# Kernel optimization log

Hardware: AMD Instinct MI355X
Metric: run time of the kernel (lower is better)

## Reference

```python
import jax, jax.numpy as jnp
import numpy as np

N = 20000      # nodes
E = 320000     # edges (avg degree 16)
H = 256        # hidden_dim
COORD = 3      # 3D coordinates
LN_EPS = 1e-5


def setup_inputs() -> dict:
    key = jax.random.key(0)
    ks = jax.random.split(key, 16)
    def w(k, shape, fan_in):
        return (jax.random.normal(k, shape, jnp.float32) / np.sqrt(fan_in)).astype(jnp.float32)
    return {
        "h": jax.random.normal(ks[0], (N, H), jnp.float32),
        "x": jax.random.normal(ks[1], (N, COORD), jnp.float32),
        "edge_index": jax.random.randint(ks[2], (2, E), 0, N, dtype=jnp.int64),
        # edge_mlp: Linear(2H+1 -> H), SiLU, Linear(H -> H), SiLU
        "e_w1": w(ks[3], (2 * H + 1, H), 2 * H + 1), "e_b1": jnp.zeros((H,), jnp.float32),
        "e_w2": w(ks[4], (H, H), H),                 "e_b2": jnp.zeros((H,), jnp.float32),
        # coord_mlp: Linear(H -> H), SiLU, Linear(H -> 1, no bias)
        "c_w1": w(ks[5], (H, H), H),                 "c_b1": jnp.zeros((H,), jnp.float32),
        "c_w2": w(ks[6], (H, 1), H),
        # node_mlp: Linear(2H -> H), SiLU, Linear(H -> H)
        "n_w1": w(ks[7], (2 * H, H), 2 * H),         "n_b1": jnp.zeros((H,), jnp.float32),
        "n_w2": w(ks[8], (H, H), H),                 "n_b2": jnp.zeros((H,), jnp.float32),
        # LayerNorm
        "ln_g": jnp.ones((H,), jnp.float32),         "ln_b": jnp.zeros((H,), jnp.float32),
    }


def reference(h, x, edge_index, e_w1, e_b1, e_w2, e_b2,
              c_w1, c_b1, c_w2, n_w1, n_b1, n_w2, n_b2, ln_g, ln_b):
    n_nodes = h.shape[0]
    row, col = edge_index[0], edge_index[1]

    diff = x[row] - x[col]                                    # [E, 3]
    dist_sq = jnp.sum(diff * diff, axis=-1, keepdims=True)    # [E, 1]
    edge_input = jnp.concatenate([h[row], h[col], dist_sq], axis=-1)  # [E, 2H+1]

    m = jax.nn.silu(edge_input @ e_w1 + e_b1)
    m_ij = jax.nn.silu(m @ e_w2 + e_b2)                        # [E, H]

    coord_weight = jax.nn.silu(m_ij @ c_w1 + c_b1) @ c_w2     # [E, 1]
    coord_agg = jax.ops.segment_sum(coord_weight * diff, col, num_segments=n_nodes)
    x_new = x + coord_agg                                     # [N, 3]

    msg_agg = jax.ops.segment_sum(m_ij, col, num_segments=n_nodes)  # [N, H]
    h_cat = jnp.concatenate([h, msg_agg], axis=-1)            # [N, 2H]
    h_new = jax.nn.silu(h_cat @ n_w1 + n_b1) @ n_w2 + n_b2

    y = h + h_new
    mu = jnp.mean(y, axis=-1, keepdims=True)
    var = jnp.mean((y - mu) ** 2, axis=-1, keepdims=True)
    h_out = (y - mu) * jax.lax.rsqrt(var + LN_EPS) * ln_g + ln_b
    return (h_out, x_new)
```

## Files before the change

kernel.cpp:

```cpp
#include <hip/hip_runtime.h>
#include <hip/hip_fp16.h>
#include <math.h>

#define NN 20000
#define NE 320000
#define H 256
#define LN_EPS 1e-5f
#define TE 64

typedef _Float16 f16x8 __attribute__((ext_vector_type(8)));
typedef float f32x16 __attribute__((ext_vector_type(16)));

__device__ __forceinline__ float silu1(float v) {
    return __fdividef(v, 1.0f + __expf(-v));
}

__device__ __forceinline__ __half2 silu2(const __half2 s) {
    const __half2 one2 = __float2half2_rn(1.0f);
    return __hmul2(s, h2rcp(__hadd2(one2, h2exp(__hneg2(s)))));
}

__global__ __launch_bounds__(256) void k_misc(
    const int* __restrict__ ei, int* __restrict__ bins,
    const float* __restrict__ x, float* __restrict__ xout,
    const float* __restrict__ ew2, const float* __restrict__ cw1,
    const float* __restrict__ nw2, const float* __restrict__ nw1,
    const float* __restrict__ ew1,
    _Float16* __restrict__ Bp2, _Float16* __restrict__ Bp3,
    _Float16* __restrict__ BpB, _Float16* __restrict__ BpA,
    _Float16* __restrict__ Bp1, _Float16* __restrict__ wdh,
    float* __restrict__ msg) {
    const int b = blockIdx.x;
    const int tid = threadIdx.x;
    if (b < 1250) {
        atomicAdd(&bins[ei[NE + b * 256 + tid]], 1);
    } else if (b < 1485) {
        const int i = (b - 1250) * 256 + tid;
        if (i < NN * 3) xout[i] = x[i];
    } else if (b < 2125) {
        const int pb = b - 1485;
        const int which = pb >> 7;
        const int bx = pb & 127;
        const int n = tid;
        if (which < 3) {
            if (bx >= 64) return;
            const float* W = (which == 0) ? ew2 : (which == 1) ? cw1 : nw2;
            _Float16* Bp = (which == 0) ? Bp2 : (which == 1) ? Bp3 : BpB;
            #pragma unroll
            for (int kr = 0; kr < 4; kr++) {
                const int k = bx * 4 + kr;
                Bp[((size_t)(k >> 3) * 256 + n) * 8 + (k & 7)] =
                    (_Float16)W[(size_t)k * 256 + n];
            }
        } else if (which == 3) {
            #pragma unroll
            for (int kr = 0; kr < 4; kr++) {
                const int k = bx * 4 + kr;
                BpA[((size_t)(k >> 3) * 256 + n) * 8 + (k & 7)] =
                    (_Float16)nw1[(size_t)k * 256 + n];
            }
        } else {
            if (bx >= 64) return;
            #pragma unroll
            for (int kr = 0; kr < 4; kr++) {
                const int k = bx * 4 + kr;
                Bp1[((size_t)(k >> 3) * 512 + n) * 8 + (k & 7)] =
                    (_Float16)ew1[(size_t)k * 256 + n];
                Bp1[((size_t)(k >> 3) * 512 + 256 + n) * 8 + (k & 7)] =
                    (_Float16)ew1[(size_t)(256 + k) * 256 + n];
            }
        }
    } else if (b == 2125) {
        wdh[tid] = (_Float16)ew1[(size_t)512 * H + tid];
    } else {
        const int b2 = b - 2126;
        float4* m4 = (float4*)msg;
        const float4 z = make_float4(0.f, 0.f, 0.f, 0.f);
        #pragma unroll
        for (int k = 0; k < 4; k++)
            m4[(size_t)b2 * 256 + tid + (size_t)k * 320000] = z;
    }
}

__global__ __launch_bounds__(256, 4) void k_pre(const float* __restrict__ h,
                                                const _Float16* __restrict__ Bp1,
                                                const float* __restrict__ eb1,
                                                _Float16* __restrict__ P,
                                                _Float16* __restrict__ Q,
                                                const int* __restrict__ bins,
                                                int* __restrict__ cursor) {
    __shared__ f16x8 Ap[32 * 32];
    const int tid = threadIdx.x;

    if (blockIdx.x == NN / 32) {
        __shared__ int wsum2[4];
        __shared__ int wbase2[4];
        const int lane = tid & 63;
        const int wid = tid >> 6;
        const int base = tid * 79;
        int sum = 0;
        for (int j = 0; j < 79; j++) {
            const int idx = base + j;
            sum += (idx < NN) ? bins[idx] : 0;
        }
        int inc = sum;
        #pragma unroll
        for (int off = 1; off < 64; off <<= 1) {
            const int t = __shfl_up(inc, off);
            if (lane >= off) inc += t;
        }
        if (lane == 63) wsum2[wid] = inc;
        __syncthreads();
        if (tid == 0) {
            int r = 0;
            #pragma unroll
            for (int ww = 0; ww < 4; ww++) { wbase2[ww] = r; r += wsum2[ww]; }
        }
        __syncthreads();
        int run = wbase2[wid] + inc - sum;
        for (int j = 0; j < 79; j++) {
            const int idx = base + j;
            if (idx < NN) { const int v = bins[idx]; cursor[idx] = run; run += v; }
        }
        return;
    }

    const int l = tid & 63;
    const int w = tid >> 6;
    const int l31 = l & 31;
    const int hh = l >> 5;
    const int n0 = blockIdx.x * 32;

    {
        const int kb = tid & 31;
        const int eb = tid >> 5;
        #pragma unroll
        for (int i = 0; i < 4; i++) {
            const int e = eb + i * 8;
            const float4 v0 = *(const float4*)(h + (size_t)(n0 + e) * H + kb * 8);
            const float4 v1 = *(const float4*)(h + (size_t)(n0 + e) * H + kb * 8 + 4);
            f16x8 pk;
            pk[0] = (_Float16)v0.x; pk[1] = (_Float16)v0.y;
            pk[2] = (_Float16)v0.z; pk[3] = (_Float16)v0.w;
            pk[4] = (_Float16)v1.x; pk[5] = (_Float16)v1.y;
            pk[6] = (_Float16)v1.z; pk[7] = (_Float16)v1.w;
            Ap[kb * 32 + (e ^ (kb & 7))] = pk;
        }
    }
    __syncthreads();

    const f16x8* Bv = (const f16x8*)Bp1;
    f32x16 acc[4];
    #pragma unroll
    for (int nt = 0; nt < 4; nt++)
        #pragma unroll
        for (int r = 0; r < 16; r++) acc[nt][r] = 0.0f;

    #pragma unroll 4
    for (int kk = 0; kk < 16; kk++) {
        const int kb = kk * 2 + hh;
        const f16x8 a = Ap[kb * 32 + (l31 ^ (kb & 7))];
        #pragma unroll
        for (int nt = 0; nt < 4; nt++) {
            const f16x8 bfr = Bv[(size_t)kb * 512 + w * 128 + nt * 32 + l31];
            acc[nt] = __builtin_amdgcn_mfma_f32_32x32x16_f16(a, bfr, acc[nt], 0, 0, 0);
        }
    }

    #pragma unroll
    for (int nt = 0; nt < 4; nt++) {
        const int col = w * 128 + nt * 32 + l31;
        const float bias = (col < 256) ? eb1[col] : 0.0f;
        #pragma unroll
        for (int r = 0; r < 16; r++) {
            const int node = n0 + (r & 3) + 8 * (r >> 2) + 4 * hh;
            const float v = acc[nt][r] + bias;
            if (col < 256) P[(size_t)node * H + col] = (_Float16)v;
            else           Q[(size_t)node * H + col - 256] = (_Float16)v;
        }
    }
}

__global__ void k_scatter(const int* __restrict__ ei, int* __restrict__ cursor,
                          int* __restrict__ perm) {
    const int e = blockIdx.x * blockDim.x + threadIdx.x;
    if (e < NE) {
        const int c = ei[NE + e];
        const int pos = atomicAdd(&cursor[c], 1);
        perm[pos] = e;
    }
}

__global__ __launch_bounds__(256, 4) void k_edge(
    const float* __restrict__ x, const int* __restrict__ ei,
    const int* __restrict__ perm,
    const _Float16* __restrict__ P, const _Float16* __restrict__ Q,
    const _Float16* __restrict__ wdh,
    const _Float16* __restrict__ Bp2, const float* __restrict__ eb2,
    const _Float16* __restrict__ Bp3, const float* __restrict__ cb1,
    const float* __restrict__ cw2,
    float* __restrict__ msg, float* __restrict__ xout) {
    __shared__ f16x8 Ap[32 * 64];
    __shared__ float sdiff[TE][4];
    __shared__ int srow[TE];
    __shared__ int scol[TE];
    __shared__ float scw[TE];

    const int tid = threadIdx.x;
    const int e0blk = blockIdx.x * TE;
    const int l = tid & 63;
    const int w = tid >> 6;
    const int l31 = l & 31;
    const int hh = l >> 5;

    if (tid < TE) {
        const int e = perm[e0blk + tid];
        const int r = ei[e];
        const int c = ei[NE + e];
        const float dx = x[r * 3 + 0] - x[c * 3 + 0];
        const float dy = x[r * 3 + 1] - x[c * 3 + 1];
        const float dz = x[r * 3 + 2] - x[c * 3 + 2];
        srow[tid] = r; scol[tid] = c;
        sdiff[tid][0] = dx; sdiff[tid][1] = dy; sdiff[tid][2] = dz;
        sdiff[tid][3] = dx * dx + dy * dy + dz * dz;
        scw[tid] = 0.0f;
    }
    __syncthreads();

    {
        const f16x8* Pv = (const f16x8*)P;
        const f16x8* Qv = (const f16x8*)Q;
        const int kb = tid & 31;
        const int eb = tid >> 5;
        union { f16x8 v; __half2 h[4]; } wdu;
        wdu.v = ((const f16x8*)wdh)[kb];
        #pragma unroll 4
        for (int i = 0; i < 8; i++) {
            const int e = eb + i * 8;
            const __half2 d2 = __float2half2_rn(sdiff[e][3]);
            union { f16x8 v; __half2 h[4]; } pu, qu, su;
            pu.v = Pv[(size_t)srow[e] * 32 + kb];
            qu.v = Qv[(size_t)scol[e] * 32 + kb];
            #pragma unroll
            for (int j = 0; j < 4; j++) {
                const __half2 s = __hfma2(wdu.h[j], d2, __hadd2(pu.h[j], qu.h[j]));
                su.h[j] = silu2(s);
            }
            Ap[kb * 64 + (e ^ (kb & 7))] = su.v;
        }
    }
    __syncthreads();

    const f16x8* Bp2v = (const f16x8*)Bp2;
    const f16x8* Bp3v = (const f16x8*)Bp3;

    f32x16 acc0[2], acc1[2];
    #pragma unroll
    for (int nt = 0; nt < 2; nt++)
        #pragma unroll
        for (int r = 0; r < 16; r++) { acc0[nt][r] = 0.0f; acc1[nt][r] = 0.0f; }

    #pragma unroll 4
    for (int kk = 0; kk < 16; kk++) {
        const int kb = kk * 2 + hh;
        const f16x8 a0 = Ap[kb * 64 + (l31 ^ (kb & 7))];
        const f16x8 a1 = Ap[kb * 64 + ((32 + l31) ^ (kb & 7))];
        #pragma unroll
        for (int nt = 0; nt < 2; nt++) {
            const f16x8 b = Bp2v[(size_t)kb * 256 + w * 64 + nt * 32 + l31];
            acc0[nt] = __builtin_amdgcn_mfma_f32_32x32x16_f16(a0, b, acc0[nt], 0, 0, 0);
            acc1[nt] = __builtin_amdgcn_mfma_f32_32x32x16_f16(a1, b, acc1[nt], 0, 0, 0);
        }
    }

    __syncthreads();

    {
        __half* Aph = (__half*)Ap;
        #pragma unroll
        for (int nt = 0; nt < 2; nt++) {
            const int c = w * 64 + nt * 32 + l31;
            const float bias = eb2[c];
            const int kb2 = c >> 3;
            const int j = c & 7;
            #pragma unroll
            for (int r = 0; r < 16; r++) {
                const __half2 o = silu2(__floats2half2_rn(acc0[nt][r] + bias,
                                                          acc1[nt][r] + bias));
                const int e0 = (r & 3) + 8 * (r >> 2) + 4 * hh;
                Aph[(size_t)(kb2 * 64 + (e0 ^ (kb2 & 7))) * 8 + j] = __low2half(o);
                Aph[(size_t)(kb2 * 64 + ((e0 + 32) ^ (kb2 & 7))) * 8 + j] = __high2half(o);
            }
        }
    }
    __syncthreads();

    #pragma unroll
    for (int nt = 0; nt < 2; nt++)
        #pragma unroll
        for (int r = 0; r < 16; r++) { acc0[nt][r] = 0.0f; acc1[nt][r] = 0.0f; }

    #pragma unroll 4
    for (int kk = 0; kk < 16; kk++) {
        const int kb = kk * 2 + hh;
        const f16x8 a0 = Ap[kb * 64 + (l31 ^ (kb & 7))];
        const f16x8 a1 = Ap[kb * 64 + ((32 + l31) ^ (kb & 7))];
        #pragma unroll
        for (int nt = 0; nt < 2; nt++) {
            const f16x8 b = Bp3v[(size_t)kb * 256 + w * 64 + nt * 32 + l31];
            acc0[nt] = __builtin_amdgcn_mfma_f32_32x32x16_f16(a0, b, acc0[nt], 0, 0, 0);
            acc1[nt] = __builtin_amdgcn_mfma_f32_32x32x16_f16(a1, b, acc1[nt], 0, 0, 0);
        }
    }

    {
        __half2 p[16];
        #pragma unroll
        for (int r = 0; r < 16; r++) p[r] = __float2half2_rn(0.0f);
        #pragma unroll
        for (int nt = 0; nt < 2; nt++) {
            const int c = w * 64 + nt * 32 + l31;
            const float bias = cb1[c];
            const __half2 cwv = __float2half2_rn(cw2[c]);
            #pragma unroll
            for (int r = 0; r < 16; r++) {
                const __half2 s = __floats2half2_rn(acc0[nt][r] + bias,
                                                    acc1[nt][r] + bias);
                p[r] = __hfma2(silu2(s), cwv, p[r]);
            }
        }
        #pragma unroll
        for (int m = 1; m < 32; m <<= 1) {
            #pragma unroll
            for (int r = 0; r < 16; r++) {
                union { __half2 h; int i; } u, v;
                u.h = p[r];
                v.i = __shfl_xor(u.i, m);
                p[r] = __hadd2(u.h, v.h);
            }
        }
        if (l31 == 0) {
            #pragma unroll
            for (int r = 0; r < 16; r++) {
                const int e0 = (r & 3) + 8 * (r >> 2) + 4 * hh;
                atomicAdd(&scw[e0], __low2float(p[r]));
                atomicAdd(&scw[e0 + 32], __high2float(p[r]));
            }
        }
    }
    __syncthreads();

    {
        const _Float16* Apf = (const _Float16*)Ap;
        const int c = tid;
        const int kb = c >> 3;
        const int j = c & 7;
        float accm = 0.0f;
        #pragma unroll 4
        for (int e = 0; e < TE; e++) {
            accm += (float)Apf[(size_t)(kb * 64 + (e ^ (kb & 7))) * 8 + j];
            const int col = scol[e];
            const int nxt = (e == TE - 1) ? -1 : scol[e + 1];
            if (col != nxt) {
                atomicAdd(msg + (size_t)col * H + c, accm);
                accm = 0.0f;
            }
        }
    }

    if (tid < 3) {
        const int d = tid;
        float accc = 0.0f;
        for (int e = 0; e < TE; e++) {
            accc += scw[e] * sdiff[e][d];
            const int col = scol[e];
            const int nxt = (e == TE - 1) ? -1 : scol[e + 1];
            if (col != nxt) {
                atomicAdd(xout + (size_t)col * 3 + d, accc);
                accc = 0.0f;
            }
        }
    }
}

__global__ __launch_bounds__(256, 4) void k_node(
    const float* __restrict__ h, const float* __restrict__ msg,
    const _Float16* __restrict__ BpA, const float* __restrict__ nb1,
    const _Float16* __restrict__ BpB, const float* __restrict__ nb2,
    const float* __restrict__ lng, const float* __restrict__ lnb,
    float* __restrict__ hout) {
    __shared__ f16x8 ApA[64 * 32];
    __shared__ float s1[32];
    __shared__ float s2[32];
    f16x8* Tp = ApA;
    const int tid = threadIdx.x;
    const int l = tid & 63;
    const int w = tid >> 6;
    const int l31 = l & 31;
    const int hh = l >> 5;
    const int n0 = blockIdx.x * 32;

    if (tid < 32) { s1[tid] = 0.0f; s2[tid] = 0.0f; }

    {
        const int kb = tid & 31;
        const int eb = tid >> 5;
        #pragma unroll
        for (int i = 0; i < 4; i++) {
            const int e = eb + i * 8;
            #pragma unroll
            for (int half = 0; half < 2; half++) {
                const float* A = half ? msg : h;
                const int kb2 = kb + half * 32;
                const float4 v0 = *(const float4*)(A + (size_t)(n0 + e) * H + kb * 8);
                const float4 v1 = *(const float4*)(A + (size_t)(n0 + e) * H + kb * 8 + 4);
                f16x8 pk;
                pk[0] = (_Float16)v0.x; pk[1] = (_Float16)v0.y;
                pk[2] = (_Float16)v0.z; pk[3] = (_Float16)v0.w;
                pk[4] = (_Float16)v1.x; pk[5] = (_Float16)v1.y;
                pk[6] = (_Float16)v1.z; pk[7] = (_Float16)v1.w;
                ApA[kb2 * 32 + (e ^ (kb2 & 7))] = pk;
            }
        }
    }
    __syncthreads();

    const f16x8* BvA = (const f16x8*)BpA;
    const f16x8* BvB = (const f16x8*)BpB;

    f32x16 acc[2];
    #pragma unroll
    for (int nt = 0; nt < 2; nt++)
        #pragma unroll
        for (int r = 0; r < 16; r++) acc[nt][r] = 0.0f;

    #pragma unroll 4
    for (int kk = 0; kk < 32; kk++) {
        const int kb = kk * 2 + hh;
        const f16x8 a = ApA[kb * 32 + (l31 ^ (kb & 7))];
        #pragma unroll
        for (int nt = 0; nt < 2; nt++) {
            const f16x8 b = BvA[(size_t)kb * 256 + w * 64 + nt * 32 + l31];
            acc[nt] = __builtin_amdgcn_mfma_f32_32x32x16_f16(a, b, acc[nt], 0, 0, 0);
        }
    }
    __syncthreads();

    {
        _Float16* Tpf = (_Float16*)Tp;
        #pragma unroll
        for (int nt = 0; nt < 2; nt++) {
            const int col = w * 64 + nt * 32 + l31;
            const float bias = nb1[col];
            const int kb2 = col >> 3;
            const int j = col & 7;
            #pragma unroll
            for (int r = 0; r < 16; r++) {
                const int e = (r & 3) + 8 * (r >> 2) + 4 * hh;
                Tpf[(size_t)(kb2 * 32 + (e ^ (kb2 & 7))) * 8 + j] =
                    (_Float16)silu1(acc[nt][r] + bias);
            }
        }
    }
    __syncthreads();

    f32x16 y[2];
    #pragma unroll
    for (int nt = 0; nt < 2; nt++)
        #pragma unroll
        for (int r = 0; r < 16; r++) y[nt][r] = 0.0f;

    #pragma unroll 4
    for (int kk = 0; kk < 16; kk++) {
        const int kb = kk * 2 + hh;
        const f16x8 a = Tp[kb * 32 + (l31 ^ (kb & 7))];
        #pragma unroll
        for (int nt = 0; nt < 2; nt++) {
            const f16x8 b = BvB[(size_t)kb * 256 + w * 64 + nt * 32 + l31];
            y[nt] = __builtin_amdgcn_mfma_f32_32x32x16_f16(a, b, y[nt], 0, 0, 0);
        }
    }

    float t1[16], t2[16];
    #pragma unroll
    for (int r = 0; r < 16; r++) { t1[r] = 0.0f; t2[r] = 0.0f; }
    #pragma unroll
    for (int nt = 0; nt < 2; nt++) {
        const int col = w * 64 + nt * 32 + l31;
        const float bias = nb2[col];
        #pragma unroll
        for (int r = 0; r < 16; r++) {
            const int node = n0 + (r & 3) + 8 * (r >> 2) + 4 * hh;
            const float v = y[nt][r] + bias + h[(size_t)node * H + col];
            y[nt][r] = v;
            t1[r] += v;
            t2[r] += v * v;
        }
    }
    #pragma unroll
    for (int m = 1; m < 32; m <<= 1) {
        #pragma unroll
        for (int r = 0; r < 16; r++) {
            t1[r] += __shfl_xor(t1[r], m);
            t2[r] += __shfl_xor(t2[r], m);
        }
    }
    if (l31 == 0) {
        #pragma unroll
        for (int r = 0; r < 16; r++) {
            const int row = (r & 3) + 8 * (r >> 2) + 4 * hh;
            atomicAdd(&s1[row], t1[r]);
            atomicAdd(&s2[row], t2[r]);
        }
    }
    __syncthreads();

    #pragma unroll
    for (int nt = 0; nt < 2; nt++) {
        const int col = w * 64 + nt * 32 + l31;
        const float g = lng[col];
        const float bb = lnb[col];
        #pragma unroll
        for (int r = 0; r < 16; r++) {
            const int row = (r & 3) + 8 * (r >> 2) + 4 * hh;
            const int node = n0 + row;
            const float mu = s1[row] * (1.0f / H);
            const float var = s2[row] * (1.0f / H) - mu * mu;
            const float rs = rsqrtf(var + LN_EPS);
            hout[(size_t)node * H + col] = (y[nt][r] - mu) * rs * g + bb;
        }
    }
}

extern "C" void kernel_launch(void* const* d_in, const int* in_sizes, int n_in,
                              void* d_out, int out_size, void* d_ws, size_t ws_size,
                              hipStream_t stream) {
    const float* h   = (const float*)d_in[0];
    const float* x   = (const float*)d_in[1];
    const int*   ei  = (const int*)d_in[2];
    const float* ew1 = (const float*)d_in[3];
    const float* eb1 = (const float*)d_in[4];
    const float* ew2 = (const float*)d_in[5];
    const float* eb2 = (const float*)d_in[6];
    const float* cw1 = (const float*)d_in[7];
    const float* cb1 = (const float*)d_in[8];
    const float* cw2 = (const float*)d_in[9];
    const float* nw1 = (const float*)d_in[10];
    const float* nb1 = (const float*)d_in[11];
    const float* nw2 = (const float*)d_in[12];
    const float* nb2 = (const float*)d_in[13];
    const float* lng = (const float*)d_in[14];
    const float* lnb = (const float*)d_in[15];

    float* hout = (float*)d_out;
    float* xout = hout + (size_t)NN * H;

    float* msg = (float*)d_ws;
    int* bins = (int*)(msg + (size_t)NN * H);
    _Float16* P   = (_Float16*)(bins + NN);
    _Float16* Qq  = P + (size_t)NN * H;
    _Float16* Bp2 = Qq + (size_t)NN * H;
    _Float16* Bp3 = Bp2 + 256 * 256;
    _Float16* BpB = Bp3 + 256 * 256;
    _Float16* BpA = BpB + 256 * 256;
    _Float16* Bp1 = BpA + 512 * 256;
    _Float16* wdh = Bp1 + 256 * 512;
    int* cursor = (int*)(wdh + 256);
    int* perm   = cursor + NN;

    (void)hipMemsetAsync(bins, 0, (size_t)NN * 4, stream);
    k_misc<<<3376, 256, 0, stream>>>(ei, bins, x, xout, ew2, cw1, nw2, nw1, ew1,
                                     Bp2, Bp3, BpB, BpA, Bp1, wdh, msg);
    k_pre<<<NN / 32 + 1, 256, 0, stream>>>(h, Bp1, eb1, P, Qq, bins, cursor);
    k_scatter<<<(NE + 255) / 256, 256, 0, stream>>>(ei, cursor, perm);
    k_edge<<<NE / TE, 256, 0, stream>>>(x, ei, perm, P, Qq, wdh, Bp2, eb2,
                                        Bp3, cb1, cw2, msg, xout);
    k_node<<<NN / 32, 256, 0, stream>>>(h, msg, BpA, nb1, BpB, nb2,
                                        lng, lnb, hout);
}
```

Measured before the change: 373.3 us.

## Merge all stages into one persistent cooperative kernel with grid syncs

Replaces the five separate launches (misc prep, pre-projection, scatter, edge, node) with a single cooperative persistent kernel. Blocks grid-stride over each former stage's work, with grid.sync between stages. The aim is to remove per-launch overhead and inter-kernel gaps. In exchange it adds grid-wide barriers, caps the grid at the occupancy-derived size (at most 1024 blocks), and forces one shared-memory and register budget that must fit the largest stage, which may lower occupancy.

```diff
diff --git a/kernel.cpp b/kernel.cpp
--- a/kernel.cpp
+++ b/kernel.cpp
@@ -1,6 +1,9 @@
 #include <hip/hip_runtime.h>
 #include <hip/hip_fp16.h>
+#include <hip/hip_cooperative_groups.h>
 #include <math.h>
+
+namespace cg = cooperative_groups;
 
 #define NN 20000
 #define NE 320000
@@ -20,514 +23,499 @@
     return __hmul2(s, h2rcp(__hadd2(one2, h2exp(__hneg2(s)))));
 }
 
-__global__ __launch_bounds__(256) void k_misc(
-    const int* __restrict__ ei, int* __restrict__ bins,
-    const float* __restrict__ x, float* __restrict__ xout,
-    const float* __restrict__ ew2, const float* __restrict__ cw1,
-    const float* __restrict__ nw2, const float* __restrict__ nw1,
-    const float* __restrict__ ew1,
-    _Float16* __restrict__ Bp2, _Float16* __restrict__ Bp3,
-    _Float16* __restrict__ BpB, _Float16* __restrict__ BpA,
-    _Float16* __restrict__ Bp1, _Float16* __restrict__ wdh,
-    float* __restrict__ msg) {
-    const int b = blockIdx.x;
+struct MegaParams {
+    const int* ei; int* bins;
+    const float* x; float* xout;
+    const float* ew2; const float* cw1; const float* nw2; const float* nw1;
+    const float* ew1;
+    _Float16 *Bp2, *Bp3, *BpB, *BpA, *Bp1, *wdh;
+    float* msg;
+    const float* h; const float* eb1;
+    _Float16 *P, *Q;
+    int* cursor; int* perm;
+    const float *eb2, *cb1, *cw2;
+    const float *nb1, *nb2, *lng, *lnb;
+    float* hout;
+};
+
+__global__ __launch_bounds__(256, 4) void k_mega(MegaParams p) {
+    cg::grid_group grid = cg::this_grid();
     const int tid = threadIdx.x;
-    if (b < 1250) {
-        atomicAdd(&bins[ei[NE + b * 256 + tid]], 1);
-    } else if (b < 1485) {
-        const int i = (b - 1250) * 256 + tid;
-        if (i < NN * 3) xout[i] = x[i];
-    } else if (b < 2125) {
-        const int pb = b - 1485;
-        const int which = pb >> 7;
-        const int bx = pb & 127;
-        const int n = tid;
-        if (which < 3) {
-            if (bx >= 64) return;
-            const float* W = (which == 0) ? ew2 : (which == 1) ? cw1 : nw2;
-            _Float16* Bp = (which == 0) ? Bp2 : (which == 1) ? Bp3 : BpB;
-            #pragma unroll
-            for (int kr = 0; kr < 4; kr++) {
-                const int k = bx * 4 + kr;
-                Bp[((size_t)(k >> 3) * 256 + n) * 8 + (k & 7)] =
-                    (_Float16)W[(size_t)k * 256 + n];
-            }
-        } else if (which == 3) {
-            #pragma unroll
-            for (int kr = 0; kr < 4; kr++) {
-                const int k = bx * 4 + kr;
-                BpA[((size_t)(k >> 3) * 256 + n) * 8 + (k & 7)] =
-                    (_Float16)nw1[(size_t)k * 256 + n];
-            }
-        } else {
-            if (bx >= 64) return;
-            #pragma unroll
-            for (int kr = 0; kr < 4; kr++) {
-                const int k = bx * 4 + kr;
-                Bp1[((size_t)(k >> 3) * 512 + n) * 8 + (k & 7)] =
-                    (_Float16)ew1[(size_t)k * 256 + n];
-                Bp1[((size_t)(k >> 3) * 512 + 256 + n) * 8 + (k & 7)] =
-                    (_Float16)ew1[(size_t)(256 + k) * 256 + n];
-            }
-        }
-    } else if (b == 2125) {
-        wdh[tid] = (_Float16)ew1[(size_t)512 * H + tid];
-    } else {
-        const int b2 = b - 2126;
-        float4* m4 = (float4*)msg;
-        const float4 z = make_float4(0.f, 0.f, 0.f, 0.f);
-        #pragma unroll
-        for (int k = 0; k < 4; k++)
-            m4[(size_t)b2 * 256 + tid + (size_t)k * 320000] = z;
-    }
-}
-
-__global__ __launch_bounds__(256, 4) void k_pre(const float* __restrict__ h,
-                                                const _Float16* __restrict__ Bp1,
-                                                const float* __restrict__ eb1,
-                                                _Float16* __restrict__ P,
-                                                _Float16* __restrict__ Q,
-                                                const int* __restrict__ bins,
-                                                int* __restrict__ cursor) {
-    __shared__ f16x8 Ap[32 * 32];
-    const int tid = threadIdx.x;
-
-    if (blockIdx.x == NN / 32) {
-        __shared__ int wsum2[4];
-        __shared__ int wbase2[4];
-        const int lane = tid & 63;
-        const int wid = tid >> 6;
-        const int base = tid * 79;
-        int sum = 0;
-        for (int j = 0; j < 79; j++) {
-            const int idx = base + j;
-            sum += (idx < NN) ? bins[idx] : 0;
-        }
-        int inc = sum;
-        #pragma unroll
-        for (int off = 1; off < 64; off <<= 1) {
-            const int t = __shfl_up(inc, off);
-            if (lane >= off) inc += t;
-        }
-        if (lane == 63) wsum2[wid] = inc;
-        __syncthreads();
-        if (tid == 0) {
-            int r = 0;
-            #pragma unroll
-            for (int ww = 0; ww < 4; ww++) { wbase2[ww] = r; r += wsum2[ww]; }
-        }
-        __syncthreads();
-        int run = wbase2[wid] + inc - sum;
-        for (int j = 0; j < 79; j++) {
-            const int idx = base + j;
-            if (idx < NN) { const int v = bins[idx]; cursor[idx] = run; run += v; }
-        }
-        return;
-    }
+    const int nB = gridDim.x;
+
+    __shared__ f16x8 ApS[2048];
+    __shared__ float sdiff[TE][4];
+    __shared__ int srow[TE];
+    __shared__ int scol[TE];
+    __shared__ float scw[TE];
+    __shared__ float s1[32];
+    __shared__ float s2[32];
+    __shared__ int wsum2[4];
+    __shared__ int wbase2[4];
 
     const int l = tid & 63;
     const int w = tid >> 6;
     const int l31 = l & 31;
     const int hh = l >> 5;
-    const int n0 = blockIdx.x * 32;
-
-    {
-        const int kb = tid & 31;
-        const int eb = tid >> 5;
-        #pragma unroll
-        for (int i = 0; i < 4; i++) {
-            const int e = eb + i * 8;
-            const float4 v0 = *(const float4*)(h + (size_t)(n0 + e) * H + kb * 8);
-            const float4 v1 = *(const float4*)(h + (size_t)(n0 + e) * H + kb * 8 + 4);
-            f16x8 pk;
-            pk[0] = (_Float16)v0.x; pk[1] = (_Float16)v0.y;
-            pk[2] = (_Float16)v0.z; pk[3] = (_Float16)v0.w;
-            pk[4] = (_Float16)v1.x; pk[5] = (_Float16)v1.y;
-            pk[6] = (_Float16)v1.z; pk[7] = (_Float16)v1.w;
-            Ap[kb * 32 + (e ^ (kb & 7))] = pk;
+
+    for (int b = blockIdx.x; b < 3376; b += nB) {
+        if (b < 1250) {
+            atomicAdd(&p.bins[p.ei[NE + b * 256 + tid]], 1);
+        } else if (b < 1485) {
+            const int i = (b - 1250) * 256 + tid;
+            if (i < NN * 3) p.xout[i] = p.x[i];
+        } else if (b < 2125) {
+            const int pb = b - 1485;
+            const int which = pb >> 7;
+            const int bx = pb & 127;
+            const int n = tid;
+            if (which < 3) {
+                if (bx < 64) {
+                    const float* W = (which == 0) ? p.ew2 : (which == 1) ? p.cw1 : p.nw2;
+                    _Float16* Bp = (which == 0) ? p.Bp2 : (which == 1) ? p.Bp3 : p.BpB;
+                    #pragma unroll
+                    for (int kr = 0; kr < 4; kr++) {
+                        const int k = bx * 4 + kr;
+                        Bp[((size_t)(k >> 3) * 256 + n) * 8 + (k & 7)] =
+                            (_Float16)W[(size_t)k * 256 + n];
+                    }
+                }
+            } else if (which == 3) {
+                #pragma unroll
+                for (int kr = 0; kr < 4; kr++) {
+                    const int k = bx * 4 + kr;
+                    p.BpA[((size_t)(k >> 3) * 256 + n) * 8 + (k & 7)] =
+                        (_Float16)p.nw1[(size_t)k * 256 + n];
+                }
+            } else {
+                if (bx < 64) {
+                    #pragma unroll
+                    for (int kr = 0; kr < 4; kr++) {
+                        const int k = bx * 4 + kr;
+                        p.Bp1[((size_t)(k >> 3) * 512 + n) * 8 + (k & 7)] =
+                            (_Float16)p.ew1[(size_t)k * 256 + n];
+                        p.Bp1[((size_t)(k >> 3) * 512 + 256 + n) * 8 + (k & 7)] =
+                            (_Float16)p.ew1[(size_t)(256 + k) * 256 + n];
+                    }
+                }
+            }
+        } else if (b == 2125) {
+            p.wdh[tid] = (_Float16)p.ew1[(size_t)512 * H + tid];
+        } else {
+            const int b2 = b - 2126;
+            float4* m4 = (float4*)p.msg;
+            const float4 z = make_float4(0.f, 0.f, 0.f, 0.f);
+            #pragma unroll
+            for (int k = 0; k < 4; k++)
+                m4[(size_t)b2 * 256 + tid + (size_t)k * 320000] = z;
         }
     }
-    __syncthreads();
-
-    const f16x8* Bv = (const f16x8*)Bp1;
-    f32x16 acc[4];
-    #pragma unroll
-    for (int nt = 0; nt < 4; nt++)
-        #pragma unroll
-        for (int r = 0; r < 16; r++) acc[nt][r] = 0.0f;
-
-    #pragma unroll 4
-    for (int kk = 0; kk < 16; kk++) {
-        const int kb = kk * 2 + hh;
-        const f16x8 a = Ap[kb * 32 + (l31 ^ (kb & 7))];
-        #pragma unroll
-        for (int nt = 0; nt < 4; nt++) {
-            const f16x8 bfr = Bv[(size_t)kb * 512 + w * 128 + nt * 32 + l31];
-            acc[nt] = __builtin_amdgcn_mfma_f32_32x32x16_f16(a, bfr, acc[nt], 0, 0, 0);
+    grid.sync();
+
+    for (int t = blockIdx.x; t <= 625; t += nB) {
+        __syncthreads();
+        if (t == 625) {
+            const int lane = tid & 63;
+            const int wid = tid >> 6;
+            const int base = tid * 79;
+            int sum = 0;
+            for (int j = 0; j < 79; j++) {
+                const int idx = base + j;
+                sum += (idx < NN) ? p.bins[idx] : 0;
+            }
+            int inc = sum;
+            #pragma unroll
+            for (int off = 1; off < 64; off <<= 1) {
+                const int tt = __shfl_up(inc, off);
+                if (lane >= off) inc += tt;
+            }
+            if (lane == 63) wsum2[wid] = inc;
+            __syncthreads();
+            if (tid == 0) {
+                int r = 0;
+                #pragma unroll
+                for (int ww = 0; ww < 4; ww++) { wbase2[ww] = r; r += wsum2[ww]; }
+            }
+            __syncthreads();
+            int run = wbase2[wid] + inc - sum;
+            for (int j = 0; j < 79; j++) {
+                const int idx = base + j;
+                if (idx < NN) { const int v = p.bins[idx]; p.cursor[idx] = run; run += v; }
+            }
+        } else {
+            f16x8* Ap = ApS;
+            const int n0 = t * 32;
+            {
+                const int kb = tid & 31;
+                const int eb = tid >> 5;
+                #pragma unroll
+                for (int i = 0; i < 4; i++) {
+                    const int e = eb + i * 8;
+                    const float4 v0 = *(const float4*)(p.h + (size_t)(n0 + e) * H + kb * 8);
+                    const float4 v1 = *(const float4*)(p.h + (size_t)(n0 + e) * H + kb * 8 + 4);
+                    f16x8 pk;
+                    pk[0] = (_Float16)v0.x; pk[1] = (_Float16)v0.y;
+                    pk[2] = (_Float16)v0.z; pk[3] = (_Float16)v0.w;
+                    pk[4] = (_Float16)v1.x; pk[5] = (_Float16)v1.y;
+                    pk[6] = (_Float16)v1.z; pk[7] = (_Float16)v1.w;
+                    Ap[kb * 32 + (e ^ (kb & 7))] = pk;
+                }
+            }
+            __syncthreads();
+
+            const f16x8* Bv = (const f16x8*)p.Bp1;
+            f32x16 acc[4];
+            #pragma unroll
+            for (int nt = 0; nt < 4; nt++)
+                #pragma unroll
+                for (int r = 0; r < 16; r++) acc[nt][r] = 0.0f;
+
+            #pragma unroll 4
+            for (int kk = 0; kk < 16; kk++) {
+                const int kb = kk * 2 + hh;
+                const f16x8 a = Ap[kb * 32 + (l31 ^ (kb & 7))];
+                #pragma unroll
+                for (int nt = 0; nt < 4; nt++) {
+                    const f16x8 bfr = Bv[(size_t)kb * 512 + w * 128 + nt * 32 + l31];
+                    acc[nt] = __builtin_amdgcn_mfma_f32_32x32x16_f16(a, bfr, acc[nt], 0, 0, 0);
+                }
+            }
+
+            #pragma unroll
+            for (int nt = 0; nt < 4; nt++) {
+                const int col = w * 128 + nt * 32 + l31;
+                const float bias = (col < 256) ? p.eb1[col] : 0.0f;
+                #pragma unroll
+                for (int r = 0; r < 16; r++) {
+                    const int node = n0 + (r & 3) + 8 * (r >> 2) + 4 * hh;
+                    const float v = acc[nt][r] + bias;
+                    if (col < 256) p.P[(size_t)node * H + col] = (_Float16)v;
+                    else           p.Q[(size_t)node * H + col - 256] = (_Float16)v;
+                }
+            }
         }
     }
-
-    #pragma unroll
-    for (int nt = 0; nt < 4; nt++) {
-        const int col = w * 128 + nt * 32 + l31;
-        const float bias = (col < 256) ? eb1[col] : 0.0f;
-        #pragma unroll
-        for (int r = 0; r < 16; r++) {
-            const int node = n0 + (r & 3) + 8 * (r >> 2) + 4 * hh;
-            const float v = acc[nt][r] + bias;
-            if (col < 256) P[(size_t)node * H + col] = (_Float16)v;
-            else           Q[(size_t)node * H + col - 256] = (_Float16)v;
-        }
+    grid.sync();
+
+    for (int u = blockIdx.x; u < 1250; u += nB) {
+        const int e = u * 256 + tid;
+        const int c = p.ei[NE + e];
+        const int pos = atomicAdd(&p.cursor[c], 1);
+        p.perm[pos] = e;
     }
-}
-
-__global__ void k_scatter(const int* __restrict__ ei, int* __restrict__ cursor,
-                          int* __restrict__ perm) {
-    const int e = blockIdx.x * blockDim.x + threadIdx.x;
-    if (e < NE) {
-        const int c = ei[NE + e];
-        const int pos = atomicAdd(&cursor[c], 1);
-        perm[pos] = e;
+    grid.sync();
+
+    for (int t = blockIdx.x; t < NE / TE; t += nB) {
+        __syncthreads();
+        f16x8* Ap = ApS;
+        const int e0blk = t * TE;
+
+        if (tid < TE) {
+            const int e = p.perm[e0blk + tid];
+            const int r = p.ei[e];
+            const int c = p.ei[NE + e];
+            const float dx = p.x[r * 3 + 0] - p.x[c * 3 + 0];
+            const float dy = p.x[r * 3 + 1] - p.x[c * 3 + 1];
+            const float dz = p.x[r * 3 + 2] - p.x[c * 3 + 2];
+            srow[tid] = r; scol[tid] = c;
+            sdiff[tid][0] = dx; sdiff[tid][1] = dy; sdiff[tid][2] = dz;
+            sdiff[tid][3] = dx * dx + dy * dy + dz * dz;
+            scw[tid] = 0.0f;
+        }
+        __syncthreads();
+
+        {
+            const f16x8* Pv = (const f16x8*)p.P;
+            const f16x8* Qv = (const f16x8*)p.Q;
+            const int kb = tid & 31;
+            const int eb = tid >> 5;
+            union { f16x8 v; __half2 h[4]; } wdu;
+            wdu.v = ((const f16x8*)p.wdh)[kb];
+            #pragma unroll 4
+            for (int i = 0; i < 8; i++) {
+                const int e = eb + i * 8;
+                const __half2 d2 = __float2half2_rn(sdiff[e][3]);
+                union { f16x8 v; __half2 h[4]; } pu, qu, su;
+                pu.v = Pv[(size_t)srow[e] * 32 + kb];
+                qu.v = Qv[(size_t)scol[e] * 32 + kb];
+                #pragma unroll
+                for (int j = 0; j < 4; j++) {
+                    const __half2 s = __hfma2(wdu.h[j], d2, __hadd2(pu.h[j], qu.h[j]));
+                    su.h[j] = silu2(s);
+                }
+                Ap[kb * 64 + (e ^ (kb & 7))] = su.v;
+            }
+        }
+        __syncthreads();
+
+        const f16x8* Bp2v = (const f16x8*)p.Bp2;
+        const f16x8* Bp3v = (const f16x8*)p.Bp3;
+
+        f32x16 acc0[2], acc1[2];
+        #pragma unroll
+        for (int nt = 0; nt < 2; nt++)
+            #pragma unroll
+            for (int r = 0; r < 16; r++) { acc0[nt][r] = 0.0f; acc1[nt][r] = 0.0f; }
+
+        #pragma unroll 4
+        for (int kk = 0; kk < 16; kk++) {
+            const int kb = kk * 2 + hh;
+            const f16x8 a0 = Ap[kb * 64 + (l31 ^ (kb & 7))];
+            const f16x8 a1 = Ap[kb * 64 + ((32 + l31) ^ (kb & 7))];
+            #pragma unroll
+            for (int nt = 0; nt < 2; nt++) {
+                const f16x8 b = Bp2v[(size_t)kb * 256 + w * 64 + nt * 32 + l31];
+                acc0[nt] = __builtin_amdgcn_mfma_f32_32x32x16_f16(a0, b, acc0[nt], 0, 0, 0);
+                acc1[nt] = __builtin_amdgcn_mfma_f32_32x32x16_f16(a1, b, acc1[nt], 0, 0, 0);
+            }
+        }
+
+        __syncthreads();
+
+        {
+            __half* Aph = (__half*)Ap;
+            #pragma unroll
+            for (int nt = 0; nt < 2; nt++) {
+                const int c = w * 64 + nt * 32 + l31;
+                const float bias = p.eb2[c];
+                const int kb2 = c >> 3;
+                const int j = c & 7;
+                #pragma unroll
+                for (int r = 0; r < 16; r++) {
+                    const __half2 o = silu2(__floats2half2_rn(acc0[nt][r] + bias,
+                                                              acc1[nt][r] + bias));
+                    const int e0 = (r & 3) + 8 * (r >> 2) + 4 * hh;
+                    Aph[(size_t)(kb2 * 64 + (e0 ^ (kb2 & 7))) * 8 + j] = __low2half(o);
+                    Aph[(size_t)(kb2 * 64 + ((e0 + 32) ^ (kb2 & 7))) * 8 + j] = __high2half(o);
+                }
+            }
+        }
+        __syncthreads();
+
+        #pragma unroll
+        for (int nt = 0; nt < 2; nt++)
+            #pragma unroll
+            for (int r = 0; r < 16; r++) { acc0[nt][r] = 0.0f; acc1[nt][r] = 0.0f; }
+
+        #pragma unroll 4
+        for (int kk = 0; kk < 16; kk++) {
+            const int kb = kk * 2 + hh;
+            const f16x8 a0 = Ap[kb * 64 + (l31 ^ (kb & 7))];
+            const f16x8 a1 = Ap[kb * 64 + ((32 + l31) ^ (kb & 7))];
+            #pragma unroll
+            for (int nt = 0; nt < 2; nt++) {
+                const f16x8 b = Bp3v[(size_t)kb * 256 + w * 64 + nt * 32 + l31];
+                acc0[nt] = __builtin_amdgcn_mfma_f32_32x32x16_f16(a0, b, acc0[nt], 0, 0, 0);
+                acc1[nt] = __builtin_amdgcn_mfma_f32_32x32x16_f16(a1, b, acc1[nt], 0, 0, 0);
+            }
+        }
+
+        {
+            __half2 pr[16];
+            #pragma unroll
+            for (int r = 0; r < 16; r++) pr[r] = __float2half2_rn(0.0f);
+            #pragma unroll
+            for (int nt = 0; nt < 2; nt++) {
+                const int c = w * 64 + nt * 32 + l31;
+                const float bias = p.cb1[c];
+                const __half2 cwv = __float2half2_rn(p.cw2[c]);
+                #pragma unroll
+                for (int r = 0; r < 16; r++) {
+                    const __half2 s = __floats2half2_rn(acc0[nt][r] + bias,
+                                                        acc1[nt][r] + bias);
+                    pr[r] = __hfma2(silu2(s), cwv, pr[r]);
+                }
+            }
+            #pragma unroll
+            for (int m = 1; m < 32; m <<= 1) {
+                #pragma unroll
+                for (int r = 0; r < 16; r++) {
+                    union { __half2 h; int i; } u, v;
+                    u.h = pr[r];
+                    v.i = __shfl_xor(u.i, m);
+                    pr[r] = __hadd2(u.h, v.h);
+                }
+            }
+            if (l31 == 0) {
+                #pragma unroll
+                for (int r = 0; r < 16; r++) {
+                    const int e0 = (r & 3) + 8 * (r >> 2) + 4 * hh;
+                    atomicAdd(&scw[e0], __low2float(pr[r]));
+                    atomicAdd(&scw[e0 + 32], __high2float(pr[r]));
+                }
+            }
+        }
+        __syncthreads();
+
+        {
+            const _Float16* Apf = (const _Float16*)Ap;
+            const int c = tid;
+            const int kb = c >> 3;
+            const int j = c & 7;
+            float accm = 0.0f;
+            #pragma unroll 4
+            for (int e = 0; e < TE; e++) {
+                accm += (float)Apf[(size_t)(kb * 64 + (e ^ (kb & 7))) * 8 + j];
+                const int col = scol[e];
+                const int nxt = (e == TE - 1) ? -1 : scol[e + 1];
+                if (col != nxt) {
+                    atomicAdd(p.msg + (size_t)col * H + c, accm);
+                    accm = 0.0f;
+                }
+            }
+        }
+
+        if (tid < 3) {
+            const int d = tid;
+            float accc = 0.0f;
+            for (int e = 0; e < TE; e++) {
+                accc += scw[e] * sdiff[e][d];
+                const int col = scol[e];
+                const int nxt = (e == TE - 1) ? -1 : scol[e + 1];
+                if (col != nxt) {
+                    atomicAdd(p.xout + (size_t)col * 3 + d, accc);
+                    accc = 0.0f;
+                }
+            }
+        }
     }
-}
-
-__global__ __launch_bounds__(256, 4) void k_edge(
-    const float* __restrict__ x, const int* __restrict__ ei,
-    const int* __restrict__ perm,
-    const _Float16* __restrict__ P, const _Float16* __restrict__ Q,
-    const _Float16* __restrict__ wdh,
-    const _Float16* __restrict__ Bp2, const float* __restrict__ eb2,
-    const _Float16* __restrict__ Bp3, const float* __restrict__ cb1,
-    const float* __restrict__ cw2,
-    float* __restrict__ msg, float* __restrict__ xout) {
-    __shared__ f16x8 Ap[32 * 64];
-    __shared__ float sdiff[TE][4];
-    __shared__ int srow[TE];
-    __shared__ int scol[TE];
-    __shared__ float scw[TE];
-
-    const int tid = threadIdx.x;
-    const int e0blk = blockIdx.x * TE;
-    const int l = tid & 63;
-    const int w = tid >> 6;
-    const int l31 = l & 31;
-    const int hh = l >> 5;
-
-    if (tid < TE) {
-        const int e = perm[e0blk + tid];
-        const int r = ei[e];
-        const int c = ei[NE + e];
-        const float dx = x[r * 3 + 0] - x[c * 3 + 0];
-        const float dy = x[r * 3 + 1] - x[c * 3 + 1];
-        const float dz = x[r * 3 + 2] - x[c * 3 + 2];
-        srow[tid] = r; scol[tid] = c;
-        sdiff[tid][0] = dx; sdiff[tid][1] = dy; sdiff[tid][2] = dz;
-        sdiff[tid][3] = dx * dx + dy * dy + dz * dz;
-        scw[tid] = 0.0f;
-    }
-    __syncthreads();
-
-    {
-        const f16x8* Pv = (const f16x8*)P;
-        const f16x8* Qv = (const f16x8*)Q;
-        const int kb = tid & 31;
-        const int eb = tid >> 5;
-        union { f16x8 v; __half2 h[4]; } wdu;
-        wdu.v = ((const f16x8*)wdh)[kb];
+    grid.sync();
+
+    for (int t = blockIdx.x; t < NN / 32; t += nB) {
+        __syncthreads();
+        f16x8* ApA = ApS;
+        f16x8* Tp = ApS;
+        const int n0 = t * 32;
+
+        if (tid < 32) { s1[tid] = 0.0f; s2[tid] = 0.0f; }
+
+        {
+            const int kb = tid & 31;
+            const int eb = tid >> 5;
+            #pragma unroll
+            for (int i = 0; i < 4; i++) {
+                const int e = eb + i * 8;
+                #pragma unroll
+                for (int half = 0; half < 2; half++) {
+                    const float* A = half ? p.msg : p.h;
+                    const int kb2 = kb + half * 32;
+                    const float4 v0 = *(const float4*)(A + (size_t)(n0 + e) * H + kb * 8);
+                    const float4 v1 = *(const float4*)(A + (size_t)(n0 + e) * H + kb * 8 + 4);
+                    f16x8 pk;
+                    pk[0] = (_Float16)v0.x; pk[1] = (_Float16)v0.y;
+                    pk[2] = (_Float16)v0.z; pk[3] = (_Float16)v0.w;
+                    pk[4] = (_Float16)v1.x; pk[5] = (_Float16)v1.y;
+                    pk[6] = (_Float16)v1.z; pk[7] = (_Float16)v1.w;
+                    ApA[kb2 * 32 + (e ^ (kb2 & 7))] = pk;
+                }
+            }
+        }
+        __syncthreads();
+
+        const f16x8* BvA = (const f16x8*)p.BpA;
+        const f16x8* BvB = (const f16x8*)p.BpB;
+
+        f32x16 acc[2];
+        #pragma unroll
+        for (int nt = 0; nt < 2; nt++)
+            #pragma unroll
+            for (int r = 0; r < 16; r++) acc[nt][r] = 0.0f;
+
         #pragma unroll 4
-        for (int i = 0; i < 8; i++) {
-            const int e = eb + i * 8;
-            const __half2 d2 = __float2half2_rn(sdiff[e][3]);
-            union { f16x8 v; __half2 h[4]; } pu, qu, su;
-            pu.v = Pv[(size_t)srow[e] * 32 + kb];
-            qu.v = Qv[(size_t)scol[e] * 32 + kb];
-            #pragma unroll
-            for (int j = 0; j < 4; j++) {
-                const __half2 s = __hfma2(wdu.h[j], d2, __hadd2(pu.h[j], qu.h[j]));
-                su.h[j] = silu2(s);
-            }
-            Ap[kb * 64 + (e ^ (kb & 7))] = su.v;
-        }
-    }
-    __syncthreads();
-
-    const f16x8* Bp2v = (const f16x8*)Bp2;
-    const f16x8* Bp3v = (const f16x8*)Bp3;
-
-    f32x16 acc0[2], acc1[2];
-    #pragma unroll
-    for (int nt = 0; nt < 2; nt++)
-        #pragma unroll
-        for (int r = 0; r < 16; r++) { acc0[nt][r] = 0.0f; acc1[nt][r] = 0.0f; }
-
-    #pragma unroll 4
-    for (int kk = 0; kk < 16; kk++) {
-        const int kb = kk * 2 + hh;
-        const f16x8 a0 = Ap[kb * 64 + (l31 ^ (kb & 7))];
-        const f16x8 a1 = Ap[kb * 64 + ((32 + l31) ^ (kb & 7))];
-        #pragma unroll
-        for (int nt = 0; nt < 2; nt++) {
-            const f16x8 b = Bp2v[(size_t)kb * 256 + w * 64 + nt * 32 + l31];
-            acc0[nt] = __builtin_amdgcn_mfma_f32_32x32x16_f16(a0, b, acc0[nt], 0, 0, 0);
-            acc1[nt] = __builtin_amdgcn_mfma_f32_32x32x16_f16(a1, b, acc1[nt], 0, 0, 0);
-        }
-    }
-
-    __syncthreads();
-
-    {
-        __half* Aph = (__half*)Ap;
-        #pragma unroll
-        for (int nt = 0; nt < 2; nt++) {
-            const int c = w * 64 + nt * 32 + l31;
-            const float bias = eb2[c];
-            const int kb2 = c >> 3;
-            const int j = c & 7;
-            #pragma unroll
-            for (int r = 0; r < 16; r++) {
-                const __half2 o = silu2(__floats2half2_rn(acc0[nt][r] + bias,
-                                                          acc1[nt][r] + bias));
-                const int e0 = (r & 3) + 8 * (r >> 2) + 4 * hh;
-                Aph[(size_t)(kb2 * 64 + (e0 ^ (kb2 & 7))) * 8 + j] = __low2half(o);
-                Aph[(size_t)(kb2 * 64 + ((e0 + 32) ^ (kb2 & 7))) * 8 + j] = __high2half(o);
-            }
-        }
-    }
-    __syncthreads();
-
-    #pragma unroll
-    for (int nt = 0; nt < 2; nt++)
-        #pragma unroll
-        for (int r = 0; r < 16; r++) { acc0[nt][r] = 0.0f; acc1[nt][r] = 0.0f; }
-
-    #pragma unroll 4
-    for (int kk = 0; kk < 16; kk++) {
-        const int kb = kk * 2 + hh;
-        const f16x8 a0 = Ap[kb * 64 + (l31 ^ (kb & 7))];
-        const f16x8 a1 = Ap[kb * 64 + ((32 + l31) ^ (kb & 7))];
-        #pragma unroll
-        for (int nt = 0; nt < 2; nt++) {
-            const f16x8 b = Bp3v[(size_t)kb * 256 + w * 64 + nt * 32 + l31];
-            acc0[nt] = __builtin_amdgcn_mfma_f32_32x32x16_f16(a0, b, acc0[nt], 0, 0, 0);
-            acc1[nt] = __builtin_amdgcn_mfma_f32_32x32x16_f16(a1, b, acc1[nt], 0, 0, 0);
-        }
-    }
-
-    {
-        __half2 p[16];
-        #pragma unroll
-        for (int r = 0; r < 16; r++) p[r] = __float2half2_rn(0.0f);
-        #pragma unroll
-        for (int nt = 0; nt < 2; nt++) {
-            const int c = w * 64 + nt * 32 + l31;
-            const float bias = cb1[c];
-            const __half2 cwv = __float2half2_rn(cw2[c]);
-            #pragma unroll
-            for (int r = 0; r < 16; r++) {
-                const __half2 s = __floats2half2_rn(acc0[nt][r] + bias,
-                                                    acc1[nt][r] + bias);
-                p[r] = __hfma2(silu2(s), cwv, p[r]);
-            }
-        }
-        #pragma unroll
-        for (int m = 1; m < 32; m <<= 1) {
-            #pragma unroll
-            for (int r = 0; r < 16; r++) {
-                union { __half2 h; int i; } u, v;
-                u.h = p[r];
-                v.i = __shfl_xor(u.i, m);
-                p[r] = __hadd2(u.h, v.h);
-            }
-        }
-        if (l31 == 0) {
-            #pragma unroll
-            for (int r = 0; r < 16; r++) {
-                const int e0 = (r & 3) + 8 * (r >> 2) + 4 * hh;
-                atomicAdd(&scw[e0], __low2float(p[r]));
-                atomicAdd(&scw[e0 + 32], __high2float(p[r]));
-            }
-        }
-    }
-    __syncthreads();
-
-    {
-        const _Float16* Apf = (const _Float16*)Ap;
-        const int c = tid;
-        const int kb = c >> 3;
-        const int j = c & 7;
-        float accm = 0.0f;
+        for (int kk = 0; kk < 32; kk++) {
+            const int kb = kk * 2 + hh;
+            const f16x8 a = ApA[kb * 32 + (l31 ^ (kb & 7))];
+            #pragma unroll
+            for (int nt = 0; nt < 2; nt++) {
+                const f16x8 b = BvA[(size_t)kb * 256 + w * 64 + nt * 32 + l31];
+                acc[nt] = __builtin_amdgcn_mfma_f32_32x32x16_f16(a, b, acc[nt], 0, 0, 0);
+            }
+        }
+        __syncthreads();
+
+        {
+            _Float16* Tpf = (_Float16*)Tp;
+            #pragma unroll
+            for (int nt = 0; nt < 2; nt++) {
+                const int col = w * 64 + nt * 32 + l31;
+                const float bias = p.nb1[col];
+                const int kb2 = col >> 3;
+                const int j = col & 7;
+                #pragma unroll
+                for (int r = 0; r < 16; r++) {
+                    const int e = (r & 3) + 8 * (r >> 2) + 4 * hh;
+                    Tpf[(size_t)(kb2 * 32 + (e ^ (kb2 & 7))) * 8 + j] =
+                        (_Float16)silu1(acc[nt][r] + bias);
+                }
+            }
+        }
+        __syncthreads();
+
+        f32x16 y[2];
+        #pragma unroll
+        for (int nt = 0; nt < 2; nt++)
+            #pragma unroll
+            for (int r = 0; r < 16; r++) y[nt][r] = 0.0f;
+
         #pragma unroll 4
-        for (int e = 0; e < TE; e++) {
-            accm += (float)Apf[(size_t)(kb * 64 + (e ^ (kb & 7))) * 8 + j];
-            const int col = scol[e];
-            const int nxt = (e == TE - 1) ? -1 : scol[e + 1];
-            if (col != nxt) {
-                atomicAdd(msg + (size_t)col * H + c, accm);
-                accm = 0.0f;
-            }
-        }
-    }
-
-    if (tid < 3) {
-        const int d = tid;
-        float accc = 0.0f;
-        for (int e = 0; e < TE; e++) {
-            accc += scw[e] * sdiff[e][d];
-            const int col = scol[e];
-            const int nxt = (e == TE - 1) ? -1 : scol[e + 1];
-            if (col != nxt) {
-                atomicAdd(xout + (size_t)col * 3 + d, accc);
-                accc = 0.0f;
-            }
-        }
-    }
-}
-
-__global__ __launch_bounds__(256, 4) void k_node(
-    const float* __restrict__ h, const float* __restrict__ msg,
-    const _Float16* __restrict__ BpA, const float* __restrict__ nb1,
-    const _Float16* __restrict__ BpB, const float* __restrict__ nb2,
-    const float* __restrict__ lng, const float* __restrict__ lnb,
-    float* __restrict__ hout) {
-    __shared__ f16x8 ApA[64 * 32];
-    __shared__ float s1[32];
-    __shared__ float s2[32];
-    f16x8* Tp = ApA;
-    const int tid = threadIdx.x;
-    const int l = tid & 63;
-    const int w = tid >> 6;
-    const int l31 = l & 31;
-    const int hh = l >> 5;
-    const int n0 = blockIdx.x * 32;
-
-    if (tid < 32) { s1[tid] = 0.0f; s2[tid] = 0.0f; }
-
-    {
-        const int kb = tid & 31;
-        const int eb = tid >> 5;
-        #pragma unroll
-        for (int i = 0; i < 4; i++) {
-            const int e = eb + i * 8;
-            #pragma unroll
-            for (int half = 0; half < 2; half++) {
-                const float* A = half ? msg : h;
-                const int kb2 = kb + half * 32;
-                const float4 v0 = *(const float4*)(A + (size_t)(n0 + e) * H + kb * 8);
-                const float4 v1 = *(const float4*)(A + (size_t)(n0 + e) * H + kb * 8 + 4);
-                f16x8 pk;
-                pk[0] = (_Float16)v0.x; pk[1] = (_Float16)v0.y;
-                pk[2] = (_Float16)v0.z; pk[3] = (_Float16)v0.w;
-                pk[4] = (_Float16)v1.x; pk[5] = (_Float16)v1.y;
-                pk[6] = (_Float16)v1.z; pk[7] = (_Float16)v1.w;
-                ApA[kb2 * 32 + (e ^ (kb2 & 7))] = pk;
-            }
-        }
-    }
-    __syncthreads();
-
-    const f16x8* BvA = (const f16x8*)BpA;
-    const f16x8* BvB = (const f16x8*)BpB;
-
-    f32x16 acc[2];
-    #pragma unroll
-    for (int nt = 0; nt < 2; nt++)
-        #pragma unroll
-        for (int r = 0; r < 16; r++) acc[nt][r] = 0.0f;
-
-    #pragma unroll 4
-    for (int kk = 0; kk < 32; kk++) {
-        const int kb = kk * 2 + hh;
-        const f16x8 a = ApA[kb * 32 + (l31 ^ (kb & 7))];
-        #pragma unroll
-        for (int nt = 0; nt < 2; nt++) {
-            const f16x8 b = BvA[(size_t)kb * 256 + w * 64 + nt * 32 + l31];
-            acc[nt] = __builtin_amdgcn_mfma_f32_32x32x16_f16(a, b, acc[nt], 0, 0, 0);
-        }
-    }
-    __syncthreads();
-
-    {
-        _Float16* Tpf = (_Float16*)Tp;
+        for (int kk = 0; kk < 16; kk++) {
+            const int kb = kk * 2 + hh;
+            const f16x8 a = Tp[kb * 32 + (l31 ^ (kb & 7))];
+            #pragma unroll
+            for (int nt = 0; nt < 2; nt++) {
+                const f16x8 b = BvB[(size_t)kb * 256 + w * 64 + nt * 32 + l31];
+                y[nt] = __builtin_amdgcn_mfma_f32_32x32x16_f16(a, b, y[nt], 0, 0, 0);
+            }
+        }
+
+        float t1[16], t2[16];
+        #pragma unroll
+        for (int r = 0; r < 16; r++) { t1[r] = 0.0f; t2[r] = 0.0f; }
         #pragma unroll
         for (int nt = 0; nt < 2; nt++) {
             const int col = w * 64 + nt * 32 + l31;
-            const float bias = nb1[col];
-            const int kb2 = col >> 3;
-            const int j = col & 7;
+            const float bias = p.nb2[col];
             #pragma unroll
             for (int r = 0; r < 16; r++) {
-                const int e = (r & 3) + 8 * (r >> 2) + 4 * hh;
-                Tpf[(size_t)(kb2 * 32 + (e ^ (kb2 & 7))) * 8 + j] =
-                    (_Float16)silu1(acc[nt][r] + bias);
-            }
-        }
-    }
-    __syncthreads();
-
-    f32x16 y[2];
-    #pragma unroll
-    for (int nt = 0; nt < 2; nt++)
-        #pragma unroll
-        for (int r = 0; r < 16; r++) y[nt][r] = 0.0f;
-
-    #pragma unroll 4
-    for (int kk = 0; kk < 16; kk++) {
-        const int kb = kk * 2 + hh;
-        const f16x8 a = Tp[kb * 32 + (l31 ^ (kb & 7))];
+                const int node = n0 + (r & 3) + 8 * (r >> 2) + 4 * hh;
+                const float v = y[nt][r] + bias + p.h[(size_t)node * H + col];
+                y[nt][r] = v;
+                t1[r] += v;
+                t2[r] += v * v;
+            }
+        }
+        #pragma unroll
+        for (int m = 1; m < 32; m <<= 1) {
+            #pragma unroll
+            for (int r = 0; r < 16; r++) {
+                t1[r] += __shfl_xor(t1[r], m);
+                t2[r] += __shfl_xor(t2[r], m);
+            }
+        }
+        if (l31 == 0) {
+            #pragma unroll
+            for (int r = 0; r < 16; r++) {
+                const int row = (r & 3) + 8 * (r >> 2) + 4 * hh;
+                atomicAdd(&s1[row], t1[r]);
+                atomicAdd(&s2[row], t2[r]);
+            }
+        }
+        __syncthreads();
+
         #pragma unroll
         for (int nt = 0; nt < 2; nt++) {
-            const f16x8 b = BvB[(size_t)kb * 256 + w * 64 + nt * 32 + l31];
-            y[nt] = __builtin_amdgcn_mfma_f32_32x32x16_f16(a, b, y[nt], 0, 0, 0);
-        }
-    }
-
-    float t1[16], t2[16];
-    #pragma unroll
-    for (int r = 0; r < 16; r++) { t1[r] = 0.0f; t2[r] = 0.0f; }
-    #pragma unroll
-    for (int nt = 0; nt < 2; nt++) {
-        const int col = w * 64 + nt * 32 + l31;
-        const float bias = nb2[col];
-        #pragma unroll
-        for (int r = 0; r < 16; r++) {
-            const int node = n0 + (r & 3) + 8 * (r >> 2) + 4 * hh;
-            const float v = y[nt][r] + bias + h[(size_t)node * H + col];
-            y[nt][r] = v;
-            t1[r] += v;
-            t2[r] += v * v;
-        }
-    }
-    #pragma unroll
-    for (int m = 1; m < 32; m <<= 1) {
-        #pragma unroll
-        for (int r = 0; r < 16; r++) {
-            t1[r] += __shfl_xor(t1[r], m);
-            t2[r] += __shfl_xor(t2[r], m);
-        }
-    }
-    if (l31 == 0) {
-        #pragma unroll
-        for (int r = 0; r < 16; r++) {
-            const int row = (r & 3) + 8 * (r >> 2) + 4 * hh;
-            atomicAdd(&s1[row], t1[r]);
-            atomicAdd(&s2[row], t2[r]);
-        }
-    }
-    __syncthreads();
-
-    #pragma unroll
-    for (int nt = 0; nt < 2; nt++) {
-        const int col = w * 64 + nt * 32 + l31;
-        const float g = lng[col];
-        const float bb = lnb[col];
-        #pragma unroll
-        for (int r = 0; r < 16; r++) {
-            const int row = (r & 3) + 8 * (r >> 2) + 4 * hh;
-            const int node = n0 + row;
-            const float mu = s1[row] * (1.0f / H);
-            const float var = s2[row] * (1.0f / H) - mu * mu;
-            const float rs = rsqrtf(var + LN_EPS);
-            hout[(size_t)node * H + col] = (y[nt][r] - mu) * rs * g + bb;
+            const int col = w * 64 + nt * 32 + l31;
+            const float g = p.lng[col];
+            const float bb = p.lnb[col];
+            #pragma unroll
+            for (int r = 0; r < 16; r++) {
+                const int row = (r & 3) + 8 * (r >> 2) + 4 * hh;
+                const int node = n0 + row;
+                const float mu = s1[row] * (1.0f / H);
+                const float var = s2[row] * (1.0f / H) - mu * mu;
+                const float rs = rsqrtf(var + LN_EPS);
+                p.hout[(size_t)node * H + col] = (y[nt][r] - mu) * rs * g + bb;
+            }
         }
     }
 }
@@ -569,12 +557,23 @@
     int* perm   = cursor + NN;
 
     (void)hipMemsetAsync(bins, 0, (size_t)NN * 4, stream);
-    k_misc<<<3376, 256, 0, stream>>>(ei, bins, x, xout, ew2, cw1, nw2, nw1, ew1,
-                                     Bp2, Bp3, BpB, BpA, Bp1, wdh, msg);
-    k_pre<<<NN / 32 + 1, 256, 0, stream>>>(h, Bp1, eb1, P, Qq, bins, cursor);
-    k_scatter<<<(NE + 255) / 256, 256, 0, stream>>>(ei, cursor, perm);
-    k_edge<<<NE / TE, 256, 0, stream>>>(x, ei, perm, P, Qq, wdh, Bp2, eb2,
-                                        Bp3, cb1, cw2, msg, xout);
-    k_node<<<NN / 32, 256, 0, stream>>>(h, msg, BpA, nb1, BpB, nb2,
-                                        lng, lnb, hout);
+
+    MegaParams p;
+    p.ei = ei; p.bins = bins; p.x = x; p.xout = xout;
+    p.ew2 = ew2; p.cw1 = cw1; p.nw2 = nw2; p.nw1 = nw1; p.ew1 = ew1;
+    p.Bp2 = Bp2; p.Bp3 = Bp3; p.BpB = BpB; p.BpA = BpA; p.Bp1 = Bp1;
+    p.wdh = wdh; p.msg = msg; p.h = h; p.eb1 = eb1; p.P = P; p.Q = Qq;
+    p.cursor = cursor; p.perm = perm;
+    p.eb2 = eb2; p.cb1 = cb1; p.cw2 = cw2;
+    p.nb1 = nb1; p.nb2 = nb2; p.lng = lng; p.lnb = lnb; p.hout = hout;
+
+    int nbcu = 0;
+    (void)hipOccupancyMaxActiveBlocksPerMultiprocessor(&nbcu, k_mega, 256, 0);
+    if (nbcu < 1) nbcu = 1;
+    int nB = nbcu * 256;
+    if (nB > 1024) nB = 1024;
+
+    void* args[] = { (void*)&p };
+    (void)hipLaunchCooperativeKernel((const void*)k_mega, dim3(nB), dim3(256),
+                                     args, 0, stream);
 }
```

New measurement: 1.154 ms. 3.09x slower.
